# Optimization experiments

Hardware: AMD Instinct MI355X
Metric: run time of the kernel (lower is better)

## Reference

```python
import jax, jax.numpy as jnp
import numpy as np

L = 512  # lstm/hidden size
A = 1000  # num_actions
D = 512  # input size


def setup_inputs() -> dict:
    key = jax.random.key(0)
    ks = jax.random.split(key, 20)
    TB = 65536
    B = 256
    def lin(k, out_d, in_d):
        k1, k2 = jax.random.split(k)
        W = jax.random.normal(k1, (out_d, in_d), jnp.float32) / np.sqrt(in_d)
        b = jnp.zeros((out_d,), jnp.float32)
        return W, b
    W_t1, b_t1 = lin(ks[0], L, D)
    W_t2, b_t2 = lin(ks[1], L, L)
    Wih = jax.random.normal(ks[2], (4 * L, L), jnp.float32) / np.sqrt(L)
    Whh = jax.random.normal(ks[3], (4 * L, L), jnp.float32) / np.sqrt(L)
    bih = jnp.zeros((4 * L,), jnp.float32)
    bhh = jnp.zeros((4 * L,), jnp.float32)
    Wa1, ba1 = lin(ks[4], L, L)
    Wa2, ba2 = lin(ks[5], A, L)
    Wa2 = Wa2 * 0.01
    Wc1, bc1 = lin(ks[6], L, L)
    Wc2, bc2 = lin(ks[7], 1, L)
    h0 = jax.random.normal(ks[8], (B, L), jnp.float32)
    c0 = jax.random.normal(ks[9], (B, L), jnp.float32)
    x = jax.random.normal(ks[10], (TB, D), jnp.float32)
    done = jax.random.randint(ks[11], (TB,), 0, 2, jnp.int32)
    action = jax.random.randint(ks[12], (TB,), 0, A, jnp.int32)
    return {
        "x": x, "done": done, "action": action, "B": B,
        "W_t1": W_t1, "b_t1": b_t1, "W_t2": W_t2, "b_t2": b_t2,
        "Wih": Wih, "Whh": Whh, "bih": bih, "bhh": bhh,
        "Wa1": Wa1, "ba1": ba1, "Wa2": Wa2, "ba2": ba2,
        "Wc1": Wc1, "bc1": bc1, "Wc2": Wc2, "bc2": bc2,
        "h0": h0, "c0": c0,
    }


def reference(x, done, action, B, W_t1, b_t1, W_t2, b_t2, Wih, Whh, bih, bhh,
              Wa1, ba1, Wa2, ba2, Wc1, bc1, Wc2, bc2, h0, c0):
    # trunk: tanh MLP
    h = jnp.tanh(x @ W_t1.T + b_t1)
    h = jnp.tanh(h @ W_t2.T + b_t2)  # (T*B, L)
    T = h.shape[0] // B
    hs = h.reshape(T, B, L)
    ds = done.reshape(T, B).astype(jnp.float32)

    def step(carry, inp):
        hp, cp = carry
        xt, dt = inp
        m = (1.0 - dt)[:, None]  # reset state where done
        hp = hp * m
        cp = cp * m
        gates = xt @ Wih.T + bih + hp @ Whh.T + bhh  # (B, 4L)
        i, f, g, o = jnp.split(gates, 4, axis=-1)  # PyTorch gate order i,f,g,o
        c = jax.nn.sigmoid(f) * cp + jax.nn.sigmoid(i) * jnp.tanh(g)
        hn = jax.nn.sigmoid(o) * jnp.tanh(c)
        return (hn, c), hn

    (_, _), outs = jax.lax.scan(step, (h0, c0), (hs, ds))
    new_hidden = outs.reshape(T * B, L) + h  # residual LSTM

    # actor head
    a = jnp.tanh(new_hidden @ Wa1.T + ba1)
    logits = a @ Wa2.T + ba2  # (T*B, A)
    logp_all = jax.nn.log_softmax(logits, axis=-1)
    lp = jnp.take_along_axis(logp_all, action[:, None].astype(jnp.int32), axis=1)[:, 0]
    ent = -jnp.sum(jnp.exp(logp_all) * logp_all, axis=-1)

    # critic head
    ch = jnp.tanh(new_hidden @ Wc1.T + bc1)
    v = (ch @ Wc2.T + bc2)[:, 0]

    return jnp.stack([lp, ent, v])  # (3, T*B)
```

## Files before the change

### kernel.cpp

```cpp
#include <hip/hip_runtime.h>
#include <hip/hip_bf16.h>

typedef short v8s __attribute__((ext_vector_type(8)));
typedef float v4f __attribute__((ext_vector_type(4)));

#define S0R 12
#define NLEV 244
#define L2E 1.4426950408889634f

__device__ __forceinline__ float bf2f(unsigned short u) {
    union { unsigned int i; float f; } v; v.i = ((unsigned int)u) << 16; return v.f;
}
__device__ __forceinline__ unsigned short f2bf(float f) {
    union { float f; unsigned int i; } v; v.f = f;
    unsigned int x = v.i;
    return (unsigned short)((x + 0x7fffu + ((x >> 16) & 1u)) >> 16);
}
__device__ __forceinline__ float fsig(float x) {
    return __builtin_amdgcn_rcpf(1.f + __builtin_amdgcn_exp2f(-L2E * x));
}
__device__ __forceinline__ float ftanh(float x) {
    return 2.f * __builtin_amdgcn_rcpf(1.f + __builtin_amdgcn_exp2f((-2.f * L2E) * x)) - 1.f;
}

__device__ __forceinline__ void gld_lds16(const unsigned short* g, unsigned short* l) {
    __builtin_amdgcn_global_load_lds(
        (const __attribute__((address_space(1))) unsigned int*)g,
        (__attribute__((address_space(3))) unsigned int*)l, 16, 0, 0);
}

template <bool TANH>
__global__ __launch_bounds__(512, 2)
void gemm256(const unsigned short* __restrict__ Ag, const unsigned short* __restrict__ Wg,
             const float* __restrict__ b1,
             unsigned short* __restrict__ Cg, int Nreal, int Npad, int Ntiles, int Astr)
{
    __shared__ __align__(16) unsigned short As[2][256 * 64];
    __shared__ __align__(16) unsigned short Bs[2][256 * 64];

    const int tid  = threadIdx.x;
    const int w    = tid >> 6;
    const int lane = tid & 63;
    const int quad = lane >> 4;
    const int lr   = lane & 15;
    const int wm   = w >> 2;
    const int wn   = w & 3;

    const int nwg = gridDim.x;
    const int cpx = nwg >> 3;
    const int swz = (blockIdx.x & 7) * cpx + (blockIdx.x >> 3);
    const int m0  = (swz / Ntiles) * 256;
    const int n0  = (swz % Ntiles) * 256;

    const unsigned short* gA = Ag + (size_t)m0 * Astr;
    const unsigned short* gB = Wg + (size_t)n0 * 512;

    const int sr  = w * 8 + (lane >> 3);
    const int skg = (lane & 7) ^ ((lane >> 3) & 7);

    auto SA = [&](int buf, int u, int kt) {
        gld_lds16(gA + (size_t)(u * 64 + sr) * Astr + kt * 64 + skg * 8,
                  &As[buf][(u * 64 + w * 8) * 64]);
    };
    auto SB = [&](int buf, int u, int kt) {
        gld_lds16(gB + (size_t)(u * 64 + sr) * 512 + kt * 64 + skg * 8,
                  &Bs[buf][(u * 64 + w * 8) * 64]);
    };

    const int g8_0  = (quad ^ (lr & 7)) * 8;
    const int g8_1  = ((quad + 4) ^ (lr & 7)) * 8;
    const int aBase = (wm * 128 + lr) * 64;
    const int bBase = (wn * 64 + lr) * 64;

    v4f zz = {0.f, 0.f, 0.f, 0.f};
    v4f acc[8][4];
    #pragma unroll
    for (int m = 0; m < 8; ++m)
        #pragma unroll
        for (int n = 0; n < 4; ++n) acc[m][n] = zz;
    v8s Bf[4][2];

#define DSB(BUF)                                                         \
    _Pragma("unroll")                                                    \
    for (int n = 0; n < 4; ++n) {                                        \
        Bf[n][0] = *(const v8s*)&Bs[BUF][bBase + n * 1024 + g8_0];       \
        Bf[n][1] = *(const v8s*)&Bs[BUF][bBase + n * 1024 + g8_1];       \
    }

#define PH(BUF, Q, STMTS, PREBAR)                                                     \
    {                                                                                 \
        const v8s a00 = *(const v8s*)&As[BUF][aBase + ((Q)*2 + 0) * 1024 + g8_0];     \
        const v8s a01 = *(const v8s*)&As[BUF][aBase + ((Q)*2 + 0) * 1024 + g8_1];     \
        const v8s a10 = *(const v8s*)&As[BUF][aBase + ((Q)*2 + 1) * 1024 + g8_0];     \
        const v8s a11 = *(const v8s*)&As[BUF][aBase + ((Q)*2 + 1) * 1024 + g8_1];     \
        STMTS;                                                                        \
        PREBAR;                                                                       \
        __builtin_amdgcn_s_barrier();                                                 \
        asm volatile("s_waitcnt lgkmcnt(0)" ::: "memory");                            \
        __builtin_amdgcn_sched_barrier(0);                                            \
        __builtin_amdgcn_s_setprio(1);                                                \
        _Pragma("unroll")                                                             \
        for (int n = 0; n < 4; ++n) {                                                 \
            acc[(Q)*2    ][n] = __builtin_amdgcn_mfma_f32_16x16x32_bf16(a00, Bf[n][0], acc[(Q)*2    ][n], 0, 0, 0); \
            acc[(Q)*2    ][n] = __builtin_amdgcn_mfma_f32_16x16x32_bf16(a01, Bf[n][1], acc[(Q)*2    ][n], 0, 0, 0); \
            acc[(Q)*2 + 1][n] = __builtin_amdgcn_mfma_f32_16x16x32_bf16(a10, Bf[n][0], acc[(Q)*2 + 1][n], 0, 0, 0); \
            acc[(Q)*2 + 1][n] = __builtin_amdgcn_mfma_f32_16x16x32_bf16(a11, Bf[n][1], acc[(Q)*2 + 1][n], 0, 0, 0); \
        }                                                                             \
        __builtin_amdgcn_s_setprio(0);                                                \
        __builtin_amdgcn_s_barrier();                                                 \
    }

    SB(0, 0, 0); SB(0, 1, 0); SB(0, 2, 0); SB(0, 3, 0);
    SA(0, 0, 0); SA(0, 2, 0); SA(0, 1, 0); SA(0, 3, 0);
    SB(1, 0, 1); SB(1, 1, 1); SB(1, 2, 1); SB(1, 3, 1);
    SA(1, 0, 1); SA(1, 2, 1);
    asm volatile("s_waitcnt vmcnt(6)" ::: "memory");
    __builtin_amdgcn_s_barrier();

    #pragma unroll
    for (int i = 0; i < 4; ++i) {
        const bool more = (i < 3);
        const int t1 = 2 * i + 1, t2 = 2 * i + 2, t3 = 2 * i + 3;
        PH(0, 0, { DSB(0); SA(1, 1, t1); SA(1, 3, t1); }, )
        PH(0, 1, { if (more) { SB(0, 0, t2); SB(0, 1, t2); } }, )
        PH(0, 2, { if (more) { SB(0, 2, t2); SB(0, 3, t2); } }, )
        PH(0, 3, { if (more) { SA(0, 0, t2); SA(0, 2, t2); } },
           if (more) { asm volatile("s_waitcnt vmcnt(6)" ::: "memory"); }
           else      { asm volatile("s_waitcnt vmcnt(0)" ::: "memory"); } )
        PH(1, 0, { DSB(1); if (more) { SA(0, 1, t2); SA(0, 3, t2); } }, )
        PH(1, 1, { if (more) { SB(1, 0, t3); SB(1, 1, t3); } }, )
        PH(1, 2, { if (more) { SB(1, 2, t3); SB(1, 3, t3); } }, )
        PH(1, 3, { if (more) { SA(1, 0, t3); SA(1, 2, t3); } },
           if (more) { asm volatile("s_waitcnt vmcnt(6)" ::: "memory"); } )
    }
#undef PH
#undef DSB

    __syncthreads();
    unsigned short* Ct = wm ? &Bs[0][0] : &As[0][0];
    #pragma unroll
    for (int n = 0; n < 4; ++n) {
        const int nn = n0 + wn * 64 + n * 16 + lr;
        const float bias = (nn < Nreal) ? b1[nn] : 0.f;
        const int col = wn * 64 + n * 16 + lr;
        #pragma unroll
        for (int m = 0; m < 8; ++m) {
            #pragma unroll
            for (int r = 0; r < 4; ++r) {
                const int row = m * 16 + quad * 4 + r;
                float v = acc[m][n][r] + bias;
                if (TANH) v = ftanh(v);
                Ct[row * 256 + (((col >> 3) ^ (row & 7)) << 3) + (col & 7)] = f2bf(v);
            }
        }
    }
    __syncthreads();
    #pragma unroll
    for (int it = 0; it < 16; ++it) {
        const int c   = it * 512 + tid;
        const int row = c >> 5;
        const int gc  = c & 31;
        const unsigned short* src = (row < 128)
            ? &As[0][row * 256 + ((gc ^ (row & 7)) << 3)]
            : &Bs[0][(row - 128) * 256 + ((gc ^ (row & 7)) << 3)];
        v8s val = *(const v8s*)src;
        *(v8s*)&Cg[(size_t)(m0 + row) * Npad + n0 + gc * 8] = val;
    }
}

__global__ void cvt8(const float* __restrict__ src, unsigned short* __restrict__ dst)
{
    const size_t i = ((size_t)blockIdx.x * 256 + threadIdx.x) * 8;
    float4 f0 = *(const float4*)(src + i);
    float4 f1 = *(const float4*)(src + i + 4);
    unsigned short t8[8];
    t8[0]=f2bf(f0.x); t8[1]=f2bf(f0.y); t8[2]=f2bf(f0.z); t8[3]=f2bf(f0.w);
    t8[4]=f2bf(f1.x); t8[5]=f2bf(f1.y); t8[6]=f2bf(f1.z); t8[7]=f2bf(f1.w);
    *(v8s*)(dst + i) = *(const v8s*)t8;
}

__global__ void cvt_cat(const float* __restrict__ Whh, const float* __restrict__ Wih,
                        unsigned short* __restrict__ Wcat)
{
    const size_t i = ((size_t)blockIdx.x * 256 + threadIdx.x) * 8;
    const int row = (int)(i >> 10), col = (int)(i & 1023);
    const float* src = (col < 512) ? &Whh[(size_t)row * 512 + col]
                                   : &Wih[(size_t)row * 512 + (col - 512)];
    float4 f0 = *(const float4*)src;
    float4 f1 = *(const float4*)(src + 4);
    unsigned short t8[8];
    t8[0]=f2bf(f0.x); t8[1]=f2bf(f0.y); t8[2]=f2bf(f0.z); t8[3]=f2bf(f0.w);
    t8[4]=f2bf(f1.x); t8[5]=f2bf(f1.y); t8[6]=f2bf(f1.z); t8[7]=f2bf(f1.w);
    *(v8s*)(Wcat + i) = *(const v8s*)t8;
}

__global__ void wa2pad(const float* __restrict__ src, unsigned short* __restrict__ dst)
{
    const int i = blockIdx.x * 256 + threadIdx.x;
    const int row = i >> 9;
    dst[i] = (row < 1000) ? f2bf(src[(size_t)row * 512 + (i & 511)]) : (unsigned short)0;
}

__global__ void prep_misc(const float* __restrict__ bih, const float* __restrict__ bhh,
                          const float* __restrict__ ba1, const float* __restrict__ bc1,
                          float* __restrict__ bsum, float* __restrict__ bac)
{
    const int i = blockIdx.x * 256 + threadIdx.x;
    if (i < 2048) bsum[i] = bih[i] + bhh[i];
    else if (i < 3072) {
        int k = i - 2048;
        bac[k] = (k < 512) ? ba1[k] : bc1[k - 512];
    }
}

__global__ void init_state(const float* __restrict__ h0, const float* __restrict__ c0,
                           const int* __restrict__ done,
                           unsigned short* __restrict__ h_init, unsigned short* __restrict__ c_init,
                           unsigned short* __restrict__ zbuf)
{
    const int b = blockIdx.x;
    const float m = 1.f - (float)done[b];
    for (int k = threadIdx.x; k < 512; k += 256) {
        h_init[(size_t)b * 512 + k] = f2bf(h0[(size_t)b * 512 + k] * m);
        c_init[(size_t)b * 512 + k] = f2bf(c0[(size_t)b * 512 + k] * m);
        if (b == 0) zbuf[k] = 0;
    }
}

__global__ __launch_bounds__(256, 1)
void seg_prep(const int* __restrict__ done, int* __restrict__ rows,
              int* __restrict__ counts, int* __restrict__ offs,
              int* __restrict__ trows, int* __restrict__ tcnt, int* __restrict__ toffs,
              int* __restrict__ maxS, int* __restrict__ bar, int T)
{
    __shared__ unsigned int   bits[256][8];
    __shared__ unsigned short cnt[256][S0R];
    __shared__ unsigned short base[256][S0R];
    __shared__ int tot[S0R];
    __shared__ int goff[S0R];
    __shared__ int tcl[NLEV];
    __shared__ int tol[NLEV];
    __shared__ int tpos[NLEV];
    __shared__ int mxl[256];
    const int b = threadIdx.x;
    #pragma unroll
    for (int s = 0; s < S0R; ++s) cnt[b][s] = 0;
    #pragma unroll
    for (int i = 0; i < 8; ++i) bits[b][i] = 0;
    for (int l = b; l < NLEV; l += 256) { tcl[l] = 0; tpos[l] = 0; }
    __syncthreads();

    int s = 0, mx = 0;
    for (int t0 = 0; t0 < T; t0 += 8) {
        int d8[8];
        #pragma unroll
        for (int i = 0; i < 8; ++i) d8[i] = done[(t0 + i) * 256 + b];
        #pragma unroll
        for (int i = 0; i < 8; ++i) {
            const int t = t0 + i, d = d8[i];
            if (d) bits[b][t >> 5] |= (1u << (t & 31));
            s = (t == 0 || d) ? 0 : s + 1;
            if (s < S0R) { if (t != 0) cnt[b][s]++; }
            else atomicAdd(&tcl[s - S0R], 1);
            mx = mx > s ? mx : s;
        }
    }
    mxl[b] = mx;
    __syncthreads();

    if (b < S0R) {
        int tsum = 0;
        for (int bb = 0; bb < 256; ++bb) { base[bb][b] = (unsigned short)tsum; tsum += cnt[bb][b]; }
        tot[b] = tsum;
    }
    __syncthreads();
    if (b == 0) {
        int run = 256;
        for (int ss = 0; ss < S0R; ++ss) { goff[ss] = run; run += tot[ss]; }
        run = 0;
        for (int l = 0; l < NLEV; ++l) { tol[l] = run; run += tcl[l]; }
        int m = 0;
        for (int bb = 0; bb < 256; ++bb) m = m > mxl[bb] ? m : mxl[bb];
        *maxS = m;
        *bar  = 0;
    }
    __syncthreads();
    if (b < S0R) {
        counts[b] = tot[b] + (b == 0 ? 256 : 0);
        offs[b]   = (b == 0) ? 0 : goff[b];
    }
    for (int l = b; l < NLEV; l += 256) { tcnt[l] = tcl[l]; toffs[l] = tol[l]; }

    s = 0;
    for (int t = 0; t < T; ++t) {
        int d = (bits[b][t >> 5] >> (t & 31)) & 1;
        s = (t == 0 || d) ? 0 : s + 1;
        if (t == 0) {
            rows[b] = b;
        } else if (s < S0R) {
            int idx = goff[s] + (int)base[b][s];
            base[b][s]++;
            rows[idx] = t * 256 + b;
        } else {
            int idx = tol[s - S0R] + atomicAdd(&tpos[s - S0R], 1);
            trows[idx] = t * 256 + b;
        }
    }
}

__global__ __launch_bounds__(256)
void lstm_round(const int* __restrict__ rows, const int* __restrict__ counts,
                const int* __restrict__ offs, int s,
                const unsigned short* __restrict__ H2,
                const unsigned short* __restrict__ Wcat,
                const float* __restrict__ bsum,
                const unsigned short* __restrict__ h_init,
                const unsigned short* __restrict__ c_init,
                const unsigned short* __restrict__ zbuf,
                unsigned short* __restrict__ Hraw, unsigned short* __restrict__ Cst,
                unsigned short* __restrict__ Hnew)
{
    const int M = counts[s];
    if (M == 0) return;
    const int off    = offs[s];
    const int mtiles = (M + 127) >> 7;

    __shared__ __align__(16) unsigned short As[128 * 32];
    __shared__ __align__(16) unsigned short Bs[128 * 32];
    __shared__ __align__(16) unsigned short Gx[128 * 136];
    __shared__ float bls[128];
    __shared__ int rl[128];

    const int tid  = threadIdx.x;
    const int w    = tid >> 6;
    const int lane = tid & 63;
    const int quad = lane >> 4;
    const int lr   = lane & 15;
    const int wm   = w & 1, wn = w >> 1;
    const int c0   = blockIdx.x * 32;
    const int srow = lane >> 2;
    const int kblk = (lane & 3) ^ ((lane >> 3) & 3);

    if (tid < 128) bls[tid] = bsum[(tid >> 5) * 512 + c0 + (tid & 31)];

    const int br0 = w * 16 + srow;
    const int br1 = 64 + br0;
    const unsigned short* gB0 = Wcat + (size_t)((br0 >> 5) * 512 + c0 + (br0 & 31)) * 1024 + kblk * 8;
    const unsigned short* gB1 = Wcat + (size_t)((br1 >> 5) * 512 + c0 + (br1 & 31)) * 1024 + kblk * 8;
    unsigned short* lA0 = As + (w * 16) * 32;
    unsigned short* lA1 = As + (64 + w * 16) * 32;
    unsigned short* lB0 = Bs + (w * 16) * 32;
    unsigned short* lB1 = Bs + (64 + w * 16) * 32;

    const int swz = (quad ^ ((lr >> 1) & 3)) * 8;
    int aoff[4], boff[4];
    #pragma unroll
    for (int i = 0; i < 4; ++i) {
        aoff[i] = (wm * 64 + i * 16 + lr) * 32 + swz;
        boff[i] = (wn * 64 + i * 16 + lr) * 32 + swz;
    }

    for (int mt = blockIdx.y; mt < mtiles; mt += gridDim.y) {
        __syncthreads();
        if (tid < 128) {
            int li = mt * 128 + tid;
            rl[tid] = (li < M) ? rows[off + li] : -1;
        }
        __syncthreads();

        const int kbeg = (s == 0 && mt * 128 >= 256) ? 16 : 0;

        int g0r = rl[w * 16 + srow];
        int g1r = rl[64 + w * 16 + srow];
        const unsigned short* gA0h;
        const unsigned short* gA1h;
        if (s == 0) {
            gA0h = (g0r >= 0 && g0r < 256) ? h_init + (size_t)g0r * 512 + kblk * 8 : zbuf + kblk * 8;
            gA1h = (g1r >= 0 && g1r < 256) ? h_init + (size_t)g1r * 512 + kblk * 8 : zbuf + kblk * 8;
        } else {
            gA0h = (g0r >= 0) ? Hraw + (size_t)(g0r - 256) * 512 + kblk * 8 : zbuf + kblk * 8;
            gA1h = (g1r >= 0) ? Hraw + (size_t)(g1r - 256) * 512 + kblk * 8 : zbuf + kblk * 8;
        }
        const unsigned short* gA0x = (g0r >= 0) ? H2 + (size_t)g0r * 512 + kblk * 8 : zbuf + kblk * 8;
        const unsigned short* gA1x = (g1r >= 0) ? H2 + (size_t)g1r * 512 + kblk * 8 : zbuf + kblk * 8;

        v4f zz = {0.f, 0.f, 0.f, 0.f};
        v4f acc[4][4] = {{zz,zz,zz,zz},{zz,zz,zz,zz},{zz,zz,zz,zz},{zz,zz,zz,zz}};

        for (int k = kbeg; k < 32; ++k) {
            __syncthreads();
            const unsigned short* a0 = (k < 16) ? gA0h + k * 32 : gA0x + (k - 16) * 32;
            const unsigned short* a1 = (k < 16) ? gA1h + k * 32 : gA1x + (k - 16) * 32;
            gld_lds16(a0, lA0);
            gld_lds16(a1, lA1);
            gld_lds16(gB0 + k * 32, lB0);
            gld_lds16(gB1 + k * 32, lB1);
            __syncthreads();
            v8s a[4], b[4];
            #pragma unroll
            for (int i = 0; i < 4; ++i) { a[i] = *(const v8s*)&As[aoff[i]]; b[i] = *(const v8s*)&Bs[boff[i]]; }
            #pragma unroll
            for (int i = 0; i < 4; ++i)
                #pragma unroll
                for (int j = 0; j < 4; ++j)
                    acc[i][j] = __builtin_amdgcn_mfma_f32_16x16x32_bf16(a[i], b[j], acc[i][j], 0, 0, 0);
        }

        #pragma unroll
        for (int j = 0; j < 4; ++j) {
            const int nl = wn * 64 + j * 16 + lr;
            #pragma unroll
            for (int i = 0; i < 4; ++i)
                #pragma unroll
                for (int r = 0; r < 4; ++r)
                    Gx[(wm * 64 + i * 16 + quad * 4 + r) * 136 + nl] = f2bf(acc[i][j][r]);
        }
        __syncthreads();

        {
            const int rloc = tid >> 1;
            const int half = tid & 1;
            const int gr   = rl[rloc];
            if (gr >= 0) {
                #pragma unroll
                for (int ch = 0; ch < 2; ++ch) {
                    const int co = half * 16 + ch * 8;
                    const int kg = c0 + co;
                    v8s q0 = *(const v8s*)&Gx[rloc * 136 +   0 + co];
                    v8s q1 = *(const v8s*)&Gx[rloc * 136 +  32 + co];
                    v8s q2 = *(const v8s*)&Gx[rloc * 136 +  64 + co];
                    v8s q3 = *(const v8s*)&Gx[rloc * 136 +  96 + co];
                    v8s h2v = *(const v8s*)&H2[(size_t)gr * 512 + kg];
                    float cprev[8];
                    if (s == 0) {
                        if (gr < 256) {
                            v8s cv = *(const v8s*)&c_init[(size_t)gr * 512 + kg];
                            #pragma unroll
                            for (int e = 0; e < 8; ++e) cprev[e] = bf2f((unsigned short)cv[e]);
                        } else {
                            #pragma unroll
                            for (int e = 0; e < 8; ++e) cprev[e] = 0.f;
                        }
                    } else {
                        v8s cv = *(const v8s*)&Cst[(size_t)(gr - 256) * 512 + kg];
                        #pragma unroll
                        for (int e = 0; e < 8; ++e) cprev[e] = bf2f((unsigned short)cv[e]);
                    }
                    unsigned short hc[8], cc[8], hn[8];
                    #pragma unroll
                    for (int e = 0; e < 8; ++e) {
                        float gi = bf2f((unsigned short)q0[e]) + bls[ 0 + co + e];
                        float gf = bf2f((unsigned short)q1[e]) + bls[32 + co + e];
                        float gg = bf2f((unsigned short)q2[e]) + bls[64 + co + e];
                        float go = bf2f((unsigned short)q3[e]) + bls[96 + co + e];
                        float c  = fsig(gf) * cprev[e] + fsig(gi) * ftanh(gg);
                        float h  = fsig(go) * ftanh(c);
                        cc[e] = f2bf(c);
                        hc[e] = f2bf(h);
                        hn[e] = f2bf(h + bf2f((unsigned short)h2v[e]));
                    }
                    *(v8s*)&Cst[(size_t)gr * 512 + kg]  = *(const v8s*)cc;
                    *(v8s*)&Hraw[(size_t)gr * 512 + kg] = *(const v8s*)hc;
                    *(v8s*)&Hnew[(size_t)gr * 512 + kg] = *(const v8s*)hn;
                }
            }
        }
    }
}

__global__ __launch_bounds__(256, 1)
void lstm_tail(const int* __restrict__ trows, const int* __restrict__ tcnt,
               const int* __restrict__ toffs, const int* __restrict__ maxS_p,
               const unsigned short* __restrict__ H2,
               const unsigned short* __restrict__ Wcat,
               const float* __restrict__ bsum,
               unsigned short* __restrict__ Hraw, unsigned short* __restrict__ Cst,
               unsigned short* __restrict__ Hnew,
               int* __restrict__ bar)
{
    const int mS = *maxS_p;
    if (mS < S0R) return;
    __shared__ __align__(16) unsigned short Wl[32 * 1024];
    __shared__ __align__(16) unsigned short Hb[16 * 1024];
    __shared__ float Gb[16 * 32];
    __shared__ float bl[32];
    __shared__ int rl[16];
    const int j    = blockIdx.x;
    const int tid  = threadIdx.x;
    const int w    = tid >> 6;
    const int lane = tid & 63;
    const int quad = lane >> 4;
    const int lr   = lane & 15;

    if (tid < 32) bl[tid] = bsum[(tid >> 3) * 512 + j * 8 + (tid & 7)];

    for (int e = tid; e < 32 * 128; e += 256) {
        int n = e >> 7, kb = e & 127;
        int g = n >> 3, c = n & 7;
        *(v8s*)&Wl[n * 1024 + kb * 8] = *(const v8s*)&Wcat[(size_t)(g * 512 + j * 8 + c) * 1024 + kb * 8];
    }

    int target = 0;
    for (int s = S0R; s <= mS; ++s) {
        const int lev = s - S0R;
        const int M   = tcnt[lev];
        const int off = toffs[lev];
        for (int ch = 0; ch < M; ch += 16) {
            __syncthreads();
            if (tid < 16) rl[tid] = (ch + tid < M) ? trows[off + ch + tid] : -1;
            __syncthreads();
            {
                int r = tid >> 4, seg = (tid & 15) * 32;
                int gr = rl[r];
                if (gr >= 0) {
                    const unsigned short* srcH = &Hraw[(size_t)(gr - 256) * 512 + seg];
                    const unsigned short* srcX = &H2[(size_t)gr * 512 + seg];
                    #pragma unroll
                    for (int q = 0; q < 4; ++q) {
                        *(v8s*)&Hb[r * 1024 + seg + q * 8]       = *(const v8s*)(srcH + q * 8);
                        *(v8s*)&Hb[r * 1024 + 512 + seg + q * 8] = *(const v8s*)(srcX + q * 8);
                    }
                } else {
                    v8s z = {0,0,0,0,0,0,0,0};
                    #pragma unroll
                    for (int q = 0; q < 4; ++q) {
                        *(v8s*)&Hb[r * 1024 + seg + q * 8]       = z;
                        *(v8s*)&Hb[r * 1024 + 512 + seg + q * 8] = z;
                    }
                }
            }
            __syncthreads();
            if (w < 2) {
                v4f acc = {0.f, 0.f, 0.f, 0.f};
                for (int k = 0; k < 32; ++k) {
                    v8s a = *(const v8s*)&Hb[lr * 1024 + k * 32 + quad * 8];
                    v8s b = *(const v8s*)&Wl[(w * 16 + lr) * 1024 + k * 32 + quad * 8];
                    acc = __builtin_amdgcn_mfma_f32_16x16x32_bf16(a, b, acc, 0, 0, 0);
                }
                #pragma unroll
                for (int r = 0; r < 4; ++r)
                    Gb[(quad * 4 + r) * 32 + w * 16 + lr] = acc[r];
            }
            __syncthreads();
            if (tid < 128) {
                int r = tid >> 3, c = tid & 7;
                int gr = rl[r];
                if (gr >= 0) {
                    int k = j * 8 + c;
                    float gi = Gb[r * 32 +  0 + c] + bl[ 0 + c];
                    float gf = Gb[r * 32 +  8 + c] + bl[ 8 + c];
                    float gg = Gb[r * 32 + 16 + c] + bl[16 + c];
                    float go = Gb[r * 32 + 24 + c] + bl[24 + c];
                    float cp = bf2f(Cst[(size_t)(gr - 256) * 512 + k]);
                    float cc = fsig(gf) * cp + fsig(gi) * ftanh(gg);
                    float hh = fsig(go) * ftanh(cc);
                    Cst[(size_t)gr * 512 + k]  = f2bf(cc);
                    Hraw[(size_t)gr * 512 + k] = f2bf(hh);
                    Hnew[(size_t)gr * 512 + k] = f2bf(hh + bf2f(H2[(size_t)gr * 512 + k]));
                }
            }
        }
        target += 64;
        __threadfence();
        __syncthreads();
        if (tid == 0) {
            __hip_atomic_fetch_add(bar, 1, __ATOMIC_RELEASE, __HIP_MEMORY_SCOPE_AGENT);
            while (__hip_atomic_load(bar, __ATOMIC_ACQUIRE, __HIP_MEMORY_SCOPE_AGENT) < target) {}
        }
        __syncthreads();
        __threadfence();
    }
}

__global__ void head_reduce(const unsigned short* __restrict__ logits,
                            const int* __restrict__ action,
                            float* __restrict__ out, int TB)
{
    const int r = blockIdx.x * 4 + (threadIdx.x >> 6);
    const int lane = threadIdx.x & 63;
    const unsigned short* row = logits + (size_t)r * 1024;
    float m = -1e30f, Z = 0.f, S = 0.f;
    v8s v0 = *(const v8s*)&row[lane * 8];
    #pragma unroll
    for (int e = 0; e < 8; ++e) {
        float xv = bf2f((unsigned short)v0[e]);
        if (xv > m) { float sc = __builtin_amdgcn_exp2f((m - xv) * L2E); Z *= sc; S *= sc; m = xv; }
        float ev = __builtin_amdgcn_exp2f((xv - m) * L2E);
        Z += ev; S += xv * ev;
    }
    v8s v1 = *(const v8s*)&row[512 + lane * 8];
    #pragma unroll
    for (int e = 0; e < 8; ++e) {
        int c = 512 + lane * 8 + e;
        if (c < 1000) {
            float xv = bf2f((unsigned short)v1[e]);
            if (xv > m) { float sc = __builtin_amdgcn_exp2f((m - xv) * L2E); Z *= sc; S *= sc; m = xv; }
            float ev = __builtin_amdgcn_exp2f((xv - m) * L2E);
            Z += ev; S += xv * ev;
        }
    }
    #pragma unroll
    for (int offb = 32; offb > 0; offb >>= 1) {
        float m2 = __shfl_xor(m, offb);
        float Z2 = __shfl_xor(Z, offb);
        float S2 = __shfl_xor(S, offb);
        float M  = fmaxf(m, m2);
        float s1 = __builtin_amdgcn_exp2f((m - M) * L2E), s2 = __builtin_amdgcn_exp2f((m2 - M) * L2E);
        Z = Z * s1 + Z2 * s2;
        S = S * s1 + S2 * s2;
        m = M;
    }
    if (lane == 0) {
        float lse = m + 0.6931471805599453f * __builtin_amdgcn_logf(Z);
        float xa  = bf2f(row[action[r]]);
        out[r]      = xa - lse;
        out[TB + r] = lse - S / Z;
    }
}

__global__ void critic_v(const unsigned short* __restrict__ AC, const float* __restrict__ Wc2,
                         const float* __restrict__ bc2, float* __restrict__ out, int TB)
{
    const int r = blockIdx.x * 4 + (threadIdx.x >> 6);
    const int lane = threadIdx.x & 63;
    const unsigned short* row = AC + (size_t)r * 1024 + 512;
    v8s hv = *(const v8s*)&row[lane * 8];
    float4 w0 = *(const float4*)&Wc2[lane * 8];
    float4 w1 = *(const float4*)&Wc2[lane * 8 + 4];
    float s = bf2f((unsigned short)hv[0]) * w0.x + bf2f((unsigned short)hv[1]) * w0.y +
              bf2f((unsigned short)hv[2]) * w0.z + bf2f((unsigned short)hv[3]) * w0.w +
              bf2f((unsigned short)hv[4]) * w1.x + bf2f((unsigned short)hv[5]) * w1.y +
              bf2f((unsigned short)hv[6]) * w1.z + bf2f((unsigned short)hv[7]) * w1.w;
    #pragma unroll
    for (int offb = 32; offb > 0; offb >>= 1) s += __shfl_xor(s, offb);
    if (lane == 0) out[2 * TB + r] = s + bc2[0];
}

extern "C" void kernel_launch(void* const* d_in, const int* in_sizes, int n_in,
                              void* d_out, int out_size, void* d_ws, size_t ws_size,
                              hipStream_t stream)
{
    const float* x    = (const float*)d_in[0];
    const int*  done  = (const int*)d_in[1];
    const int*  action= (const int*)d_in[2];
    const float* W_t1 = (const float*)d_in[4];
    const float* b_t1 = (const float*)d_in[5];
    const float* W_t2 = (const float*)d_in[6];
    const float* b_t2 = (const float*)d_in[7];
    const float* Wih  = (const float*)d_in[8];
    const float* Whh  = (const float*)d_in[9];
    const float* bih  = (const float*)d_in[10];
    const float* bhh  = (const float*)d_in[11];
    const float* Wa1  = (const float*)d_in[12];
    const float* ba1  = (const float*)d_in[13];
    const float* Wa2  = (const float*)d_in[14];
    const float* ba2  = (const float*)d_in[15];
    const float* Wc1  = (const float*)d_in[16];
    const float* bc1  = (const float*)d_in[17];
    const float* Wc2  = (const float*)d_in[18];
    const float* bc2  = (const float*)d_in[19];
    const float* h0   = (const float*)d_in[20];
    const float* c0   = (const float*)d_in[21];
    float* out = (float*)d_out;

    const int TB = in_sizes[1];
    const int T  = TB / 256;

    const size_t MiB = 1024 * 1024;
    char* ws = (char*)d_ws;
    unsigned short* H1     = (unsigned short*)(ws);
    unsigned short* Hnew   = (unsigned short*)(ws);
    unsigned short* logits = (unsigned short*)(ws);
    unsigned short* AC1    = (unsigned short*)(ws + 128 * MiB);
    unsigned short* Cst    = (unsigned short*)(ws + 256 * MiB);
    unsigned short* H2     = (unsigned short*)(ws + 320 * MiB);
    unsigned short* Hraw   = (unsigned short*)(ws + 384 * MiB);
    unsigned short* xbf    = Hraw;
    unsigned short* Wt1b   = (unsigned short*)(ws + 448 * MiB);
    unsigned short* Wt2b   = Wt1b + 512 * 512;
    unsigned short* Wcat   = Wt2b + 512 * 512;
    unsigned short* Wacb   = Wcat + 2048 * 1024;
    unsigned short* Wa2b   = Wacb + 1024 * 512;
    unsigned short* h_init = Wa2b + 1024 * 512;
    unsigned short* c_init = h_init + 256 * 512;
    unsigned short* zbuf   = c_init + 256 * 512;
    int* rows   = (int*)(zbuf + 512);
    int* trows  = rows + 65536;
    int* counts = trows + 65536;
    int* offs   = counts + S0R;
    int* tcnt   = offs + S0R;
    int* toffs  = tcnt + NLEV;
    int* maxS   = toffs + NLEV;
    int* bar    = maxS + 1;
    float* bsum = (float*)(bar + 1);
    float* bac  = bsum + 2048;

    dim3 blk(256);
    dim3 blk5(512);

    cvt8<<<16384, blk, 0, stream>>>(x, xbf);
    cvt8<<<128,  blk, 0, stream>>>(W_t1, Wt1b);
    cvt8<<<128,  blk, 0, stream>>>(W_t2, Wt2b);
    cvt_cat<<<1024, blk, 0, stream>>>(Whh, Wih, Wcat);
    cvt8<<<128,  blk, 0, stream>>>(Wa1, Wacb);
    cvt8<<<128,  blk, 0, stream>>>(Wc1, Wacb + 512 * 512);
    wa2pad<<<2048, blk, 0, stream>>>(Wa2, Wa2b);
    prep_misc<<<12, blk, 0, stream>>>(bih, bhh, ba1, bc1, bsum, bac);
    init_state<<<256, blk, 0, stream>>>(h0, c0, done, h_init, c_init, zbuf);
    seg_prep<<<1, blk, 0, stream>>>(done, rows, counts, offs, trows, tcnt, toffs, maxS, bar, T);

    gemm256<true ><<<512, blk5, 0, stream>>>(xbf, Wt1b, b_t1, H1, 512, 512, 2, 512);
    gemm256<true ><<<512, blk5, 0, stream>>>(H1,  Wt2b, b_t2, H2, 512, 512, 2, 512);

    static const int Gs[S0R] = {256, 128, 64, 32, 16, 8, 4, 2, 1, 1, 1, 1};
    for (int s = 0; s < S0R; ++s)
        lstm_round<<<dim3(16, Gs[s]), blk, 0, stream>>>(rows, counts, offs, s, H2, Wcat, bsum,
                                                        h_init, c_init, zbuf, Hraw, Cst, Hnew);
    lstm_tail<<<64, blk, 0, stream>>>(trows, tcnt, toffs, maxS, H2, Wcat, bsum, Hraw, Cst, Hnew, bar);

    gemm256<true ><<<1024, blk5, 0, stream>>>(Hnew, Wacb, bac, AC1, 1024, 1024, 4, 512);

    gemm256<false><<<1024, blk5, 0, stream>>>(AC1, Wa2b, ba2, logits, 1000, 1024, 4, 1024);
    head_reduce<<<TB / 4, blk, 0, stream>>>(logits, action, out, TB);

    critic_v<<<TB / 4, blk, 0, stream>>>(AC1, Wc2, bc2, out, TB);
}
```

Baseline: 1.370 ms.

## Double-buffer LSTM round GEMM LDS staging with prefetch and explicit waitcnt

The per-k staging of A and B tiles in the LSTM round kernel now uses two LDS buffers carved out of one union array shared with the Gx epilogue buffer. The next k-slice is prefetched while the current one feeds the MFMAs, and explicit vmcnt waits with raw s_barrier replace the two __syncthreads. This hides global-to-LDS latency behind the matrix work, and the aliasing keeps total LDS usage flat so a launch-bounds hint of 4 blocks per CU can hold. The setprio calls raise the priority of waves issuing MFMAs. The hand-counted vmcnt value relies on the exact number of loads STG issues, so it is fragile.

```diff
diff --git a/kernel.cpp b/kernel.cpp
--- a/kernel.cpp
+++ b/kernel.cpp
@@ -308,7 +308,7 @@
     }
 }
 
-__global__ __launch_bounds__(256)
+__global__ __launch_bounds__(256, 4)
 void lstm_round(const int* __restrict__ rows, const int* __restrict__ counts,
                 const int* __restrict__ offs, int s,
                 const unsigned short* __restrict__ H2,
@@ -325,11 +325,10 @@
     const int off    = offs[s];
     const int mtiles = (M + 127) >> 7;
 
-    __shared__ __align__(16) unsigned short As[128 * 32];
-    __shared__ __align__(16) unsigned short Bs[128 * 32];
-    __shared__ __align__(16) unsigned short Gx[128 * 136];
+    __shared__ __align__(16) unsigned short U[17408];
     __shared__ float bls[128];
     __shared__ int rl[128];
+    unsigned short* const Gx = U;
 
     const int tid  = threadIdx.x;
     const int w    = tid >> 6;
@@ -347,10 +346,6 @@
     const int br1 = 64 + br0;
     const unsigned short* gB0 = Wcat + (size_t)((br0 >> 5) * 512 + c0 + (br0 & 31)) * 1024 + kblk * 8;
     const unsigned short* gB1 = Wcat + (size_t)((br1 >> 5) * 512 + c0 + (br1 & 31)) * 1024 + kblk * 8;
-    unsigned short* lA0 = As + (w * 16) * 32;
-    unsigned short* lA1 = As + (64 + w * 16) * 32;
-    unsigned short* lB0 = Bs + (w * 16) * 32;
-    unsigned short* lB1 = Bs + (64 + w * 16) * 32;
 
     const int swz = (quad ^ ((lr >> 1) & 3)) * 8;
     int aoff[4], boff[4];
@@ -384,26 +379,44 @@
         const unsigned short* gA0x = (g0r >= 0) ? H2 + (size_t)g0r * 512 + kblk * 8 : zbuf + kblk * 8;
         const unsigned short* gA1x = (g1r >= 0) ? H2 + (size_t)g1r * 512 + kblk * 8 : zbuf + kblk * 8;
 
+        auto STG = [&](int b, int k) {
+            const unsigned short* a0 = (k < 16) ? gA0h + k * 32 : gA0x + (k - 16) * 32;
+            const unsigned short* a1 = (k < 16) ? gA1h + k * 32 : gA1x + (k - 16) * 32;
+            unsigned short* base = U + b * 8192;
+            gld_lds16(a0, base + (w * 16) * 32);
+            gld_lds16(a1, base + (64 + w * 16) * 32);
+            gld_lds16(gB0 + k * 32, base + 4096 + (w * 16) * 32);
+            gld_lds16(gB1 + k * 32, base + 4096 + (64 + w * 16) * 32);
+        };
+
         v4f zz = {0.f, 0.f, 0.f, 0.f};
         v4f acc[4][4] = {{zz,zz,zz,zz},{zz,zz,zz,zz},{zz,zz,zz,zz},{zz,zz,zz,zz}};
 
+        STG(0, kbeg);
+        #pragma unroll 2
         for (int k = kbeg; k < 32; ++k) {
-            __syncthreads();
-            const unsigned short* a0 = (k < 16) ? gA0h + k * 32 : gA0x + (k - 16) * 32;
-            const unsigned short* a1 = (k < 16) ? gA1h + k * 32 : gA1x + (k - 16) * 32;
-            gld_lds16(a0, lA0);
-            gld_lds16(a1, lA1);
-            gld_lds16(gB0 + k * 32, lB0);
-            gld_lds16(gB1 + k * 32, lB1);
-            __syncthreads();
+            if (k < 31) {
+                STG((k + 1) & 1, k + 1);
+                asm volatile("s_waitcnt vmcnt(4)" ::: "memory");
+            } else {
+                asm volatile("s_waitcnt vmcnt(0)" ::: "memory");
+            }
+            __builtin_amdgcn_s_barrier();
+            __builtin_amdgcn_sched_barrier(0);
+            const unsigned short* Ab = U + (k & 1) * 8192;
+            const unsigned short* Bb = Ab + 4096;
             v8s a[4], b[4];
             #pragma unroll
-            for (int i = 0; i < 4; ++i) { a[i] = *(const v8s*)&As[aoff[i]]; b[i] = *(const v8s*)&Bs[boff[i]]; }
+            for (int i = 0; i < 4; ++i) { a[i] = *(const v8s*)&Ab[aoff[i]]; b[i] = *(const v8s*)&Bb[boff[i]]; }
+            __builtin_amdgcn_s_setprio(1);
             #pragma unroll
             for (int i = 0; i < 4; ++i)
                 #pragma unroll
                 for (int j = 0; j < 4; ++j)
                     acc[i][j] = __builtin_amdgcn_mfma_f32_16x16x32_bf16(a[i], b[j], acc[i][j], 0, 0, 0);
+            __builtin_amdgcn_s_setprio(0);
+            __builtin_amdgcn_s_barrier();
+            __builtin_amdgcn_sched_barrier(0);
         }
 
         #pragma unroll
```

Result: faster. 1.335 ms (-2.6%).
